# Optimization experiments

Hardware: AMD Instinct MI355X
Metric: run time of the kernel (lower is better)

Reference implementation:

```python
import jax, jax.numpy as jnp
import numpy as np

M, B, S, D, H = 8, 4, 512, 512, 8
HD = D // H  # head_dim = 64


def setup_inputs() -> dict:
    key = jax.random.key(0)
    k1, k2, k3 = jax.random.split(key, 3)
    x = jax.random.normal(k1, (M, B, S, D), dtype=jnp.float32)
    qkv_weight = jax.random.normal(k2, (M, D, 3 * D), dtype=jnp.float32) * 0.02
    proj_weight = jax.random.normal(k3, (M, D, D), dtype=jnp.float32) * 0.02
    return {"x": x, "qkv_weight": qkv_weight, "proj_weight": proj_weight}


def reference(x, qkv_weight, proj_weight):
    m, b, s, d = x.shape
    # model-axis batched QKV projection
    qkv = jnp.einsum('mbti,mio->mbto', x, qkv_weight)
    q, k, v = jnp.split(qkv, 3, axis=-1)
    # [m, b, h, s, hd]
    q = q.reshape(m, b, s, H, HD).transpose(0, 1, 3, 2, 4)
    k = k.reshape(m, b, s, H, HD).transpose(0, 1, 3, 2, 4)
    v = v.reshape(m, b, s, H, HD).transpose(0, 1, 3, 2, 4)
    att = jnp.einsum('mbhqd,mbhkd->mbhqk', q, k) / jnp.sqrt(jnp.float32(HD))
    causal = jnp.tril(jnp.ones((s, s), dtype=bool))
    att = jnp.where(causal, att, jnp.float32(-jnp.inf))
    att = jax.nn.softmax(att, axis=-1)
    y = jnp.einsum('mbhqk,mbhkd->mbhqd', att, v)
    y = y.transpose(0, 1, 3, 2, 4).reshape(m, b, s, d)
    return jnp.einsum('mbti,mio->mbto', y, proj_weight)
```

## Files before the change

### kernel.cpp

```cpp
#include <hip/hip_runtime.h>
#include <hip/hip_bf16.h>


typedef unsigned short u16;
typedef unsigned int u32;
typedef __attribute__((ext_vector_type(8))) short short8;
typedef __attribute__((ext_vector_type(4))) float f32x4;
typedef __attribute__((ext_vector_type(4))) unsigned short u16x4;
typedef __attribute__((ext_vector_type(8))) unsigned short u16x8;
typedef __attribute__((ext_vector_type(2))) unsigned int u32x2;

#define MFMA16(a, b, c) __builtin_amdgcn_mfma_f32_16x16x32_bf16((a), (b), (c), 0, 0, 0)

__device__ __forceinline__ u16 f2bf(float f) {
  union { __hip_bfloat16 h; u16 u; } cv;
  cv.h = __float2bfloat16(f);
  return cv.u;
}

__device__ __forceinline__ void gl_lds16(const u16* g, u16* l) {
  __builtin_amdgcn_global_load_lds(
      (const __attribute__((address_space(1))) void*)g,
      (__attribute__((address_space(3))) void*)l, 16, 0, 0);
}

__global__ __launch_bounds__(256) void xcast_kernel(const float* __restrict__ in,
                                                    u16* __restrict__ out, long n8) {
  long stride = (long)gridDim.x * 256;
  for (long i = blockIdx.x * 256L + threadIdx.x; i < n8; i += stride) {
    f32x4 a = *(const f32x4*)(in + i * 8);
    f32x4 b = *(const f32x4*)(in + i * 8 + 4);
    u16x8 o = {f2bf(a[0]), f2bf(a[1]), f2bf(a[2]), f2bf(a[3]),
               f2bf(b[0]), f2bf(b[1]), f2bf(b[2]), f2bf(b[3])};
    *(u16x8*)(out + i * 8) = o;
  }
}

__global__ __launch_bounds__(256) void wtrans_kernel(const float* __restrict__ in,
                                                     u16* __restrict__ out, int R, int C) {
  __shared__ float t[32][33];
  int m = blockIdx.z;
  const float* pin = in + (size_t)m * R * C;
  u16* pout = out + (size_t)m * R * C;
  int c0 = blockIdx.x * 32, r0 = blockIdx.y * 32;
  int tx = threadIdx.x, ty = threadIdx.y;
#pragma unroll
  for (int i = 0; i < 4; ++i) {
    int r = ty + i * 8;
    t[r][tx] = pin[(size_t)(r0 + r) * C + c0 + tx];
  }
  __syncthreads();
#pragma unroll
  for (int i = 0; i < 4; ++i) {
    int r = ty + i * 8;
    pout[(size_t)(c0 + r) * R + r0 + tx] = f2bf(t[tx][r]);
  }
}

__global__ __launch_bounds__(256) void qkv_gemm_kernel(const u16* __restrict__ XB,
                                                       const u16* __restrict__ WT,
                                                       u16* __restrict__ Q,
                                                       u16* __restrict__ K,
                                                       u16* __restrict__ VT) {
  __shared__ __attribute__((aligned(16))) u16 As[128 * 32];
  __shared__ __attribute__((aligned(16))) u16 Bs[128 * 32];
  int m = blockIdx.z;
  const u16* A = XB + (size_t)m * 2048 * 512;
  const u16* BT = WT + (size_t)m * 1536 * 512;
  int r0 = blockIdx.y * 128, c0 = blockIdx.x * 128;
  int t = threadIdx.x;
  int lane = t & 63, w = t >> 6;
  int wr = (w >> 1) * 64, wc = (w & 1) * 64;
  int fr = lane & 15, fc = lane >> 4;

  int u0 = w * 128 + lane;
  int u1 = w * 128 + 64 + lane;
  int ar0 = u0 >> 2, ak0 = (u0 & 3) * 8;
  int ar1 = u1 >> 2, ak1 = (u1 & 3) * 8;
  u16* lbase0 = &As[0] + (size_t)(w * 128) * 8;
  u16* lbase1 = &As[0] + (size_t)(w * 128 + 64) * 8;
  u16* lbb0 = &Bs[0] + (size_t)(w * 128) * 8;
  u16* lbb1 = &Bs[0] + (size_t)(w * 128 + 64) * 8;

  f32x4 acc[4][4];
#pragma unroll
  for (int i = 0; i < 4; ++i)
#pragma unroll
    for (int j = 0; j < 4; ++j) acc[i][j] = f32x4{0.f, 0.f, 0.f, 0.f};

  for (int kk = 0; kk < 512; kk += 32) {
    gl_lds16(A + (size_t)(r0 + ar0) * 512 + kk + ak0, lbase0);
    gl_lds16(A + (size_t)(r0 + ar1) * 512 + kk + ak1, lbase1);
    gl_lds16(BT + (size_t)(c0 + ar0) * 512 + kk + ak0, lbb0);
    gl_lds16(BT + (size_t)(c0 + ar1) * 512 + kk + ak1, lbb1);
    __syncthreads();
    short8 af[4], bf[4];
#pragma unroll
    for (int i = 0; i < 4; ++i) af[i] = *(const short8*)&As[(wr + i * 16 + fr) * 32 + fc * 8];
#pragma unroll
    for (int j = 0; j < 4; ++j) bf[j] = *(const short8*)&Bs[(wc + j * 16 + fr) * 32 + fc * 8];
#pragma unroll
    for (int i = 0; i < 4; ++i)
#pragma unroll
      for (int j = 0; j < 4; ++j) acc[i][j] = MFMA16(af[i], bf[j], acc[i][j]);
    __syncthreads();
  }

  int seg = c0 >> 9;
#pragma unroll
  for (int i = 0; i < 4; ++i) {
#pragma unroll
    for (int j = 0; j < 4; ++j) {
#pragma unroll
      for (int r = 0; r < 4; ++r) {
        int grow = r0 + wr + i * 16 + fc * 4 + r;
        int gcol = c0 + wc + j * 16 + fr;
        int b = grow >> 9, s = grow & 511;
        int cc = gcol & 511;
        int hh = cc >> 6, hd = cc & 63;
        size_t headoff = (size_t)((m * 4 + b) * 8 + hh) * 32768;
        u16 val = f2bf(acc[i][j][r]);
        if (seg == 0)      Q[headoff + s * 64 + hd] = val;
        else if (seg == 1) K[headoff + s * 64 + hd] = val;
        else               VT[headoff + hd * 512 + s] = val;
      }
    }
  }
}

__global__ __launch_bounds__(256) void attn_kernel(const u16* __restrict__ Qg,
                                                   const u16* __restrict__ Kg,
                                                   const u16* __restrict__ VTg,
                                                   u16* __restrict__ Yg) {
  __shared__ u16 Ks[2][64][72];
  __shared__ u16 Vs[2][64][72];
  __shared__ u16 Pl[4][16][72];
  int bid = blockIdx.x;
  int qt = bid >> 8;
  int g = bid & 255;
  int h = g & 7, mb = g >> 3;
  int t = threadIdx.x, lane = t & 63, w = t >> 6;
  int fr = lane & 15, fc = lane >> 4;
  size_t hoff = ((size_t)mb * 8 + h) * 32768;
  const u16* Q = Qg + hoff;
  const u16* K = Kg + hoff;
  const u16* V = VTg + hoff;
  int qrow = qt * 64 + w * 16 + fr;
  const float SC = 0.125f * 1.44269504088896340736f;

  short8 qf0 = *(const short8*)(Q + (size_t)qrow * 64 + fc * 8);
  short8 qf1 = *(const short8*)(Q + (size_t)qrow * 64 + 32 + fc * 8);

  f32x4 acc[4];
#pragma unroll
  for (int d = 0; d < 4; ++d) acc[d] = f32x4{0.f, 0.f, 0.f, 0.f};
  float mst = -1e30f, lst = 0.f;

  int u0 = 2 * t, u1 = 2 * t + 1;
  int kr0 = u0 >> 3, kc0 = (u0 & 7) * 8;
  int kr1 = u1 >> 3, kc1 = (u1 & 7) * 8;

  {
    u16x8 a0 = *(const u16x8*)(K + (size_t)kr0 * 64 + kc0);
    u16x8 a1 = *(const u16x8*)(K + (size_t)kr1 * 64 + kc1);
    u16x8 b0 = *(const u16x8*)(V + (size_t)kr0 * 512 + kc0);
    u16x8 b1 = *(const u16x8*)(V + (size_t)kr1 * 512 + kc1);
    *(u16x8*)&Ks[0][kr0][kc0] = a0;
    *(u16x8*)&Ks[0][kr1][kc1] = a1;
    *(u16x8*)&Vs[0][kr0][kc0] = b0;
    *(u16x8*)&Vs[0][kr1][kc1] = b1;
  }
  __syncthreads();

  for (int kt = 0; kt <= qt; ++kt) {
    int cur = kt & 1;
    bool pref = kt < qt;
    u16x8 nk0, nk1, nv0, nv1;
    if (pref) {
      int kbn = (kt + 1) * 64;
      nk0 = *(const u16x8*)(K + (size_t)(kbn + kr0) * 64 + kc0);
      nk1 = *(const u16x8*)(K + (size_t)(kbn + kr1) * 64 + kc1);
      nv0 = *(const u16x8*)(V + (size_t)kr0 * 512 + kbn + kc0);
      nv1 = *(const u16x8*)(V + (size_t)kr1 * 512 + kbn + kc1);
    }

    f32x4 st[4];
#pragma unroll
    for (int sub = 0; sub < 4; ++sub) {
      short8 kf0 = *(const short8*)&Ks[cur][sub * 16 + fr][fc * 8];
      short8 kf1 = *(const short8*)&Ks[cur][sub * 16 + fr][32 + fc * 8];
      f32x4 z = f32x4{0.f, 0.f, 0.f, 0.f};
      z = MFMA16(kf0, qf0, z);
      st[sub] = MFMA16(kf1, qf1, z);
    }

    float p[4][4];
    float mt = -3e30f;
    bool diag = (kt == qt);
    int qloc = w * 16 + fr;
#pragma unroll
    for (int sub = 0; sub < 4; ++sub)
#pragma unroll
      for (int r = 0; r < 4; ++r) {
        float v = st[sub][r] * SC;
        if (diag && (sub * 16 + fc * 4 + r) > qloc) v = -1e30f;
        p[sub][r] = v;
        mt = fmaxf(mt, v);
      }
    mt = fmaxf(mt, __shfl_xor(mt, 16));
    mt = fmaxf(mt, __shfl_xor(mt, 32));
    float mn = fmaxf(mst, mt);
    float al = __builtin_amdgcn_exp2f(mst - mn);
    mst = mn;
    float rs = 0.f;
#pragma unroll
    for (int sub = 0; sub < 4; ++sub)
#pragma unroll
      for (int r = 0; r < 4; ++r) {
        float e = __builtin_amdgcn_exp2f(p[sub][r] - mn);
        p[sub][r] = e;
        rs += e;
      }
    rs += __shfl_xor(rs, 16);
    rs += __shfl_xor(rs, 32);
    lst = lst * al + rs;
#pragma unroll
    for (int d = 0; d < 4; ++d) acc[d] *= al;

#pragma unroll
    for (int sub = 0; sub < 4; ++sub) {
      u32 lo = (u32)f2bf(p[sub][0]) | ((u32)f2bf(p[sub][1]) << 16);
      u32 hi = (u32)f2bf(p[sub][2]) | ((u32)f2bf(p[sub][3]) << 16);
      *(u32x2*)&Pl[w][fr][sub * 16 + fc * 4] = u32x2{lo, hi};
    }

#pragma unroll
    for (int dt = 0; dt < 4; ++dt)
#pragma unroll
      for (int kc = 0; kc < 2; ++kc) {
        short8 vf = *(const short8*)&Vs[cur][dt * 16 + fr][kc * 32 + fc * 8];
        short8 pb = *(const short8*)&Pl[w][fr][kc * 32 + fc * 8];
        acc[dt] = MFMA16(vf, pb, acc[dt]);
      }

    if (pref) {
      *(u16x8*)&Ks[cur ^ 1][kr0][kc0] = nk0;
      *(u16x8*)&Ks[cur ^ 1][kr1][kc1] = nk1;
      *(u16x8*)&Vs[cur ^ 1][kr0][kc0] = nv0;
      *(u16x8*)&Vs[cur ^ 1][kr1][kc1] = nv1;
    }
    __syncthreads();
  }

  float inv = 1.0f / lst;
#pragma unroll
  for (int dt = 0; dt < 4; ++dt) {
    u16x4 o = {f2bf(acc[dt][0] * inv), f2bf(acc[dt][1] * inv),
               f2bf(acc[dt][2] * inv), f2bf(acc[dt][3] * inv)};
    *(u16x4*)(Yg + ((size_t)mb * 512 + qrow) * 512 + h * 64 + dt * 16 + fc * 4) = o;
  }
}

__global__ __launch_bounds__(256) void proj_gemm_kernel(const u16* __restrict__ Y,
                                                        const u16* __restrict__ PT,
                                                        float* __restrict__ OUT) {
  __shared__ __attribute__((aligned(16))) u16 As[128 * 32];
  __shared__ __attribute__((aligned(16))) u16 Bs[128 * 32];
  int m = blockIdx.z;
  const u16* A = Y + (size_t)m * 2048 * 512;
  const u16* BT = PT + (size_t)m * 512 * 512;
  float* C = OUT + (size_t)m * 2048 * 512;
  int r0 = blockIdx.y * 128, c0 = blockIdx.x * 128;
  int t = threadIdx.x;
  int lane = t & 63, w = t >> 6;
  int wr = (w >> 1) * 64, wc = (w & 1) * 64;
  int fr = lane & 15, fc = lane >> 4;

  int u0 = w * 128 + lane;
  int u1 = w * 128 + 64 + lane;
  int ar0 = u0 >> 2, ak0 = (u0 & 3) * 8;
  int ar1 = u1 >> 2, ak1 = (u1 & 3) * 8;
  u16* lbase0 = &As[0] + (size_t)(w * 128) * 8;
  u16* lbase1 = &As[0] + (size_t)(w * 128 + 64) * 8;
  u16* lbb0 = &Bs[0] + (size_t)(w * 128) * 8;
  u16* lbb1 = &Bs[0] + (size_t)(w * 128 + 64) * 8;

  f32x4 acc[4][4];
#pragma unroll
  for (int i = 0; i < 4; ++i)
#pragma unroll
    for (int j = 0; j < 4; ++j) acc[i][j] = f32x4{0.f, 0.f, 0.f, 0.f};

  for (int kk = 0; kk < 512; kk += 32) {
    gl_lds16(A + (size_t)(r0 + ar0) * 512 + kk + ak0, lbase0);
    gl_lds16(A + (size_t)(r0 + ar1) * 512 + kk + ak1, lbase1);
    gl_lds16(BT + (size_t)(c0 + ar0) * 512 + kk + ak0, lbb0);
    gl_lds16(BT + (size_t)(c0 + ar1) * 512 + kk + ak1, lbb1);
    __syncthreads();
    short8 af[4], bf[4];
#pragma unroll
    for (int i = 0; i < 4; ++i) af[i] = *(const short8*)&As[(wr + i * 16 + fr) * 32 + fc * 8];
#pragma unroll
    for (int j = 0; j < 4; ++j) bf[j] = *(const short8*)&Bs[(wc + j * 16 + fr) * 32 + fc * 8];
#pragma unroll
    for (int i = 0; i < 4; ++i)
#pragma unroll
      for (int j = 0; j < 4; ++j) acc[i][j] = MFMA16(af[i], bf[j], acc[i][j]);
    __syncthreads();
  }
#pragma unroll
  for (int i = 0; i < 4; ++i)
#pragma unroll
    for (int j = 0; j < 4; ++j)
#pragma unroll
      for (int r = 0; r < 4; ++r) {
        int grow = r0 + wr + i * 16 + fc * 4 + r;
        int gcol = c0 + wc + j * 16 + fr;
        C[(size_t)grow * 512 + gcol] = acc[i][j][r];
      }
}

extern "C" void kernel_launch(void* const* d_in, const int* in_sizes, int n_in,
                              void* d_out, int out_size, void* d_ws, size_t ws_size,
                              hipStream_t stream) {
  const float* x = (const float*)d_in[0];
  const float* wqkv = (const float*)d_in[1];
  const float* wproj = (const float*)d_in[2];
  float* out = (float*)d_out;

  u16* p = (u16*)d_ws;
  u16* wqkvT = p;  p += (size_t)8 * 1536 * 512;
  u16* wprojT = p; p += (size_t)8 * 512 * 512;
  u16* qb = p;     p += (size_t)8388608;
  u16* kb = p;     p += (size_t)8388608;
  u16* vtb = p;    p += (size_t)8388608;
  u16* xyb = p;    p += (size_t)8388608;

  xcast_kernel<<<2048, 256, 0, stream>>>(x, xyb, (long)8 * 4 * 512 * 512 / 8);
  wtrans_kernel<<<dim3(48, 16, 8), dim3(32, 8), 0, stream>>>(wqkv, wqkvT, 512, 1536);
  wtrans_kernel<<<dim3(16, 16, 8), dim3(32, 8), 0, stream>>>(wproj, wprojT, 512, 512);
  qkv_gemm_kernel<<<dim3(12, 16, 8), 256, 0, stream>>>(xyb, wqkvT, qb, kb, vtb);
  attn_kernel<<<2048, 256, 0, stream>>>(qb, kb, vtb, xyb);
  proj_gemm_kernel<<<dim3(4, 16, 8), 256, 0, stream>>>(xyb, wprojT, out);
}
```

Before: 220.7 us.

## Double-buffer GEMM LDS tiles, enlarge to 256-row blocks, remap grid for XCD locality

Both the QKV and projection GEMMs now use 512-thread workgroups covering 256x128 output tiles, with double-buffered LDS so the next K-slice's global-to-LDS load is issued before computing the current one. The grid is flattened and block IDs are remapped so consecutive blocks of the same model index land on the same XCD, aiming for better L2 reuse. The intent is to hide load latency, cut one barrier per step, and improve cache locality. The cost is doubled LDS use and fewer, larger workgroups, which may lower occupancy.

```diff
diff --git a/kernel.cpp b/kernel.cpp
--- a/kernel.cpp
+++ b/kernel.cpp
@@ -57,30 +57,30 @@
   }
 }
 
-__global__ __launch_bounds__(256) void qkv_gemm_kernel(const u16* __restrict__ XB,
+__global__ __launch_bounds__(512) void qkv_gemm_kernel(const u16* __restrict__ XB,
                                                        const u16* __restrict__ WT,
                                                        u16* __restrict__ Q,
                                                        u16* __restrict__ K,
                                                        u16* __restrict__ VT) {
-  __shared__ __attribute__((aligned(16))) u16 As[128 * 32];
-  __shared__ __attribute__((aligned(16))) u16 Bs[128 * 32];
-  int m = blockIdx.z;
+  __shared__ __attribute__((aligned(16))) u16 As[2][256 * 32];
+  __shared__ __attribute__((aligned(16))) u16 Bs[2][128 * 32];
+  int bid = blockIdx.x;
+  int wgid = (bid & 7) * 96 + (bid >> 3);
+  int m = wgid / 96;
+  int rem = wgid % 96;
+  int r0 = (rem / 12) * 256, c0 = (rem % 12) * 128;
   const u16* A = XB + (size_t)m * 2048 * 512;
   const u16* BT = WT + (size_t)m * 1536 * 512;
-  int r0 = blockIdx.y * 128, c0 = blockIdx.x * 128;
   int t = threadIdx.x;
   int lane = t & 63, w = t >> 6;
   int wr = (w >> 1) * 64, wc = (w & 1) * 64;
   int fr = lane & 15, fc = lane >> 4;
 
-  int u0 = w * 128 + lane;
-  int u1 = w * 128 + 64 + lane;
-  int ar0 = u0 >> 2, ak0 = (u0 & 3) * 8;
-  int ar1 = u1 >> 2, ak1 = (u1 & 3) * 8;
-  u16* lbase0 = &As[0] + (size_t)(w * 128) * 8;
-  u16* lbase1 = &As[0] + (size_t)(w * 128 + 64) * 8;
-  u16* lbb0 = &Bs[0] + (size_t)(w * 128) * 8;
-  u16* lbb1 = &Bs[0] + (size_t)(w * 128 + 64) * 8;
+  int ar0 = t >> 2, ak0 = (t & 3) * 8;
+  int ar1 = (t + 512) >> 2, ak1 = ((t + 512) & 3) * 8;
+  u16* ldsA0[2] = {&As[0][(size_t)w * 64 * 8], &As[1][(size_t)w * 64 * 8]};
+  u16* ldsA1[2] = {&As[0][(size_t)(512 + w * 64) * 8], &As[1][(size_t)(512 + w * 64) * 8]};
+  u16* ldsB0[2] = {&Bs[0][(size_t)w * 64 * 8], &Bs[1][(size_t)w * 64 * 8]};
 
   f32x4 acc[4][4];
 #pragma unroll
@@ -88,21 +88,28 @@
 #pragma unroll
     for (int j = 0; j < 4; ++j) acc[i][j] = f32x4{0.f, 0.f, 0.f, 0.f};
 
-  for (int kk = 0; kk < 512; kk += 32) {
-    gl_lds16(A + (size_t)(r0 + ar0) * 512 + kk + ak0, lbase0);
-    gl_lds16(A + (size_t)(r0 + ar1) * 512 + kk + ak1, lbase1);
-    gl_lds16(BT + (size_t)(c0 + ar0) * 512 + kk + ak0, lbb0);
-    gl_lds16(BT + (size_t)(c0 + ar1) * 512 + kk + ak1, lbb1);
-    __syncthreads();
-    short8 af[4], bf[4];
-#pragma unroll
-    for (int i = 0; i < 4; ++i) af[i] = *(const short8*)&As[(wr + i * 16 + fr) * 32 + fc * 8];
-#pragma unroll
-    for (int j = 0; j < 4; ++j) bf[j] = *(const short8*)&Bs[(wc + j * 16 + fr) * 32 + fc * 8];
+  gl_lds16(A + (size_t)(r0 + ar0) * 512 + ak0, ldsA0[0]);
+  gl_lds16(A + (size_t)(r0 + ar1) * 512 + ak1, ldsA1[0]);
+  gl_lds16(BT + (size_t)(c0 + ar0) * 512 + ak0, ldsB0[0]);
+  __syncthreads();
+
+  for (int ks = 0; ks < 16; ++ks) {
+    int cur = ks & 1;
+    if (ks + 1 < 16) {
+      int kk = (ks + 1) * 32;
+      gl_lds16(A + (size_t)(r0 + ar0) * 512 + kk + ak0, ldsA0[cur ^ 1]);
+      gl_lds16(A + (size_t)(r0 + ar1) * 512 + kk + ak1, ldsA1[cur ^ 1]);
+      gl_lds16(BT + (size_t)(c0 + ar0) * 512 + kk + ak0, ldsB0[cur ^ 1]);
+    }
+    short8 af[4], bf_[4];
+#pragma unroll
+    for (int i = 0; i < 4; ++i) af[i] = *(const short8*)&As[cur][(wr + i * 16 + fr) * 32 + fc * 8];
+#pragma unroll
+    for (int j = 0; j < 4; ++j) bf_[j] = *(const short8*)&Bs[cur][(wc + j * 16 + fr) * 32 + fc * 8];
 #pragma unroll
     for (int i = 0; i < 4; ++i)
 #pragma unroll
-      for (int j = 0; j < 4; ++j) acc[i][j] = MFMA16(af[i], bf[j], acc[i][j]);
+      for (int j = 0; j < 4; ++j) acc[i][j] = MFMA16(af[i], bf_[j], acc[i][j]);
     __syncthreads();
   }
 
@@ -261,29 +268,29 @@
   }
 }
 
-__global__ __launch_bounds__(256) void proj_gemm_kernel(const u16* __restrict__ Y,
+__global__ __launch_bounds__(512) void proj_gemm_kernel(const u16* __restrict__ Y,
                                                         const u16* __restrict__ PT,
                                                         float* __restrict__ OUT) {
-  __shared__ __attribute__((aligned(16))) u16 As[128 * 32];
-  __shared__ __attribute__((aligned(16))) u16 Bs[128 * 32];
-  int m = blockIdx.z;
+  __shared__ __attribute__((aligned(16))) u16 As[2][256 * 32];
+  __shared__ __attribute__((aligned(16))) u16 Bs[2][128 * 32];
+  int bid = blockIdx.x;
+  int wgid = (bid & 7) * 32 + (bid >> 3);
+  int m = wgid / 32;
+  int rem = wgid % 32;
+  int r0 = (rem / 4) * 256, c0 = (rem % 4) * 128;
   const u16* A = Y + (size_t)m * 2048 * 512;
   const u16* BT = PT + (size_t)m * 512 * 512;
   float* C = OUT + (size_t)m * 2048 * 512;
-  int r0 = blockIdx.y * 128, c0 = blockIdx.x * 128;
   int t = threadIdx.x;
   int lane = t & 63, w = t >> 6;
   int wr = (w >> 1) * 64, wc = (w & 1) * 64;
   int fr = lane & 15, fc = lane >> 4;
 
-  int u0 = w * 128 + lane;
-  int u1 = w * 128 + 64 + lane;
-  int ar0 = u0 >> 2, ak0 = (u0 & 3) * 8;
-  int ar1 = u1 >> 2, ak1 = (u1 & 3) * 8;
-  u16* lbase0 = &As[0] + (size_t)(w * 128) * 8;
-  u16* lbase1 = &As[0] + (size_t)(w * 128 + 64) * 8;
-  u16* lbb0 = &Bs[0] + (size_t)(w * 128) * 8;
-  u16* lbb1 = &Bs[0] + (size_t)(w * 128 + 64) * 8;
+  int ar0 = t >> 2, ak0 = (t & 3) * 8;
+  int ar1 = (t + 512) >> 2, ak1 = ((t + 512) & 3) * 8;
+  u16* ldsA0[2] = {&As[0][(size_t)w * 64 * 8], &As[1][(size_t)w * 64 * 8]};
+  u16* ldsA1[2] = {&As[0][(size_t)(512 + w * 64) * 8], &As[1][(size_t)(512 + w * 64) * 8]};
+  u16* ldsB0[2] = {&Bs[0][(size_t)w * 64 * 8], &Bs[1][(size_t)w * 64 * 8]};
 
   f32x4 acc[4][4];
 #pragma unroll
@@ -291,21 +298,28 @@
 #pragma unroll
     for (int j = 0; j < 4; ++j) acc[i][j] = f32x4{0.f, 0.f, 0.f, 0.f};
 
-  for (int kk = 0; kk < 512; kk += 32) {
-    gl_lds16(A + (size_t)(r0 + ar0) * 512 + kk + ak0, lbase0);
-    gl_lds16(A + (size_t)(r0 + ar1) * 512 + kk + ak1, lbase1);
-    gl_lds16(BT + (size_t)(c0 + ar0) * 512 + kk + ak0, lbb0);
-    gl_lds16(BT + (size_t)(c0 + ar1) * 512 + kk + ak1, lbb1);
-    __syncthreads();
-    short8 af[4], bf[4];
-#pragma unroll
-    for (int i = 0; i < 4; ++i) af[i] = *(const short8*)&As[(wr + i * 16 + fr) * 32 + fc * 8];
-#pragma unroll
-    for (int j = 0; j < 4; ++j) bf[j] = *(const short8*)&Bs[(wc + j * 16 + fr) * 32 + fc * 8];
+  gl_lds16(A + (size_t)(r0 + ar0) * 512 + ak0, ldsA0[0]);
+  gl_lds16(A + (size_t)(r0 + ar1) * 512 + ak1, ldsA1[0]);
+  gl_lds16(BT + (size_t)(c0 + ar0) * 512 + ak0, ldsB0[0]);
+  __syncthreads();
+
+  for (int ks = 0; ks < 16; ++ks) {
+    int cur = ks & 1;
+    if (ks + 1 < 16) {
+      int kk = (ks + 1) * 32;
+      gl_lds16(A + (size_t)(r0 + ar0) * 512 + kk + ak0, ldsA0[cur ^ 1]);
+      gl_lds16(A + (size_t)(r0 + ar1) * 512 + kk + ak1, ldsA1[cur ^ 1]);
+      gl_lds16(BT + (size_t)(c0 + ar0) * 512 + kk + ak0, ldsB0[cur ^ 1]);
+    }
+    short8 af[4], bf_[4];
+#pragma unroll
+    for (int i = 0; i < 4; ++i) af[i] = *(const short8*)&As[cur][(wr + i * 16 + fr) * 32 + fc * 8];
+#pragma unroll
+    for (int j = 0; j < 4; ++j) bf_[j] = *(const short8*)&Bs[cur][(wc + j * 16 + fr) * 32 + fc * 8];
 #pragma unroll
     for (int i = 0; i < 4; ++i)
 #pragma unroll
-      for (int j = 0; j < 4; ++j) acc[i][j] = MFMA16(af[i], bf[j], acc[i][j]);
+      for (int j = 0; j < 4; ++j) acc[i][j] = MFMA16(af[i], bf_[j], acc[i][j]);
     __syncthreads();
   }
 #pragma unroll
@@ -339,7 +353,7 @@
   xcast_kernel<<<2048, 256, 0, stream>>>(x, xyb, (long)8 * 4 * 512 * 512 / 8);
   wtrans_kernel<<<dim3(48, 16, 8), dim3(32, 8), 0, stream>>>(wqkv, wqkvT, 512, 1536);
   wtrans_kernel<<<dim3(16, 16, 8), dim3(32, 8), 0, stream>>>(wproj, wprojT, 512, 512);
-  qkv_gemm_kernel<<<dim3(12, 16, 8), 256, 0, stream>>>(xyb, wqkvT, qb, kb, vtb);
+  qkv_gemm_kernel<<<768, 512, 0, stream>>>(xyb, wqkvT, qb, kb, vtb);
   attn_kernel<<<2048, 256, 0, stream>>>(qb, kb, vtb, xyb);
-  proj_gemm_kernel<<<dim3(4, 16, 8), 256, 0, stream>>>(xyb, wprojT, out);
-}
+  proj_gemm_kernel<<<256, 512, 0, stream>>>(xyb, wprojT, out);
+}
```

Result: no change. 219.9 us (-0.4%).

## Triple-buffer GEMM K-loop with async LDS loads, swizzle, and XCD-aware block mapping

Applied to the files above, without the earlier changes.

Rewrites the QKV and projection GEMM main loops to use three LDS buffers, prefetching two K-tiles ahead with a single barrier per iteration and explicit vmcnt waits. Global loads into LDS now use an XOR swizzle to reduce bank conflicts on the fragment reads. Blocks are launched as a 1D grid and remapped so that consecutive blocks on the same XCD share the same model index, which should improve L2 locality. The V-transposed epilogue now packs four bf16 values into one vector store. The cost is higher LDS use per block, which can lower occupancy.

```diff
diff --git a/kernel.cpp b/kernel.cpp
--- a/kernel.cpp
+++ b/kernel.cpp
@@ -62,25 +62,22 @@
                                                        u16* __restrict__ Q,
                                                        u16* __restrict__ K,
                                                        u16* __restrict__ VT) {
-  __shared__ __attribute__((aligned(16))) u16 As[128 * 32];
-  __shared__ __attribute__((aligned(16))) u16 Bs[128 * 32];
-  int m = blockIdx.z;
+  __shared__ __attribute__((aligned(16))) u16 As[3][128 * 32];
+  __shared__ __attribute__((aligned(16))) u16 Bs[3][128 * 32];
+  int bid = blockIdx.x;
+  int wgid = (bid & 7) * 192 + (bid >> 3);
+  int m = wgid / 192;
+  int rem = wgid % 192;
+  int r0 = (rem / 12) * 128, c0 = (rem % 12) * 128;
   const u16* A = XB + (size_t)m * 2048 * 512;
   const u16* BT = WT + (size_t)m * 1536 * 512;
-  int r0 = blockIdx.y * 128, c0 = blockIdx.x * 128;
   int t = threadIdx.x;
   int lane = t & 63, w = t >> 6;
   int wr = (w >> 1) * 64, wc = (w & 1) * 64;
   int fr = lane & 15, fc = lane >> 4;
 
-  int u0 = w * 128 + lane;
-  int u1 = w * 128 + 64 + lane;
-  int ar0 = u0 >> 2, ak0 = (u0 & 3) * 8;
-  int ar1 = u1 >> 2, ak1 = (u1 & 3) * 8;
-  u16* lbase0 = &As[0] + (size_t)(w * 128) * 8;
-  u16* lbase1 = &As[0] + (size_t)(w * 128 + 64) * 8;
-  u16* lbb0 = &Bs[0] + (size_t)(w * 128) * 8;
-  u16* lbb1 = &Bs[0] + (size_t)(w * 128 + 64) * 8;
+  int rA0 = t >> 2, cA0 = t & 3, sA0 = cA0 ^ ((rA0 >> 1) & 3);
+  int rA1 = (t + 256) >> 2, cA1 = t & 3, sA1 = cA1 ^ ((rA1 >> 1) & 3);
 
   f32x4 acc[4][4];
 #pragma unroll
@@ -88,43 +85,84 @@
 #pragma unroll
     for (int j = 0; j < 4; ++j) acc[i][j] = f32x4{0.f, 0.f, 0.f, 0.f};
 
-  for (int kk = 0; kk < 512; kk += 32) {
-    gl_lds16(A + (size_t)(r0 + ar0) * 512 + kk + ak0, lbase0);
-    gl_lds16(A + (size_t)(r0 + ar1) * 512 + kk + ak1, lbase1);
-    gl_lds16(BT + (size_t)(c0 + ar0) * 512 + kk + ak0, lbb0);
-    gl_lds16(BT + (size_t)(c0 + ar1) * 512 + kk + ak1, lbb1);
-    __syncthreads();
-    short8 af[4], bf[4];
-#pragma unroll
-    for (int i = 0; i < 4; ++i) af[i] = *(const short8*)&As[(wr + i * 16 + fr) * 32 + fc * 8];
-#pragma unroll
-    for (int j = 0; j < 4; ++j) bf[j] = *(const short8*)&Bs[(wc + j * 16 + fr) * 32 + fc * 8];
+#define QKV_STAGE(tile)                                                          \
+  {                                                                              \
+    int kk_ = (tile) * 32;                                                       \
+    int b_ = (tile) % 3;                                                         \
+    gl_lds16(A + (size_t)(r0 + rA0) * 512 + kk_ + sA0 * 8, &As[b_][w * 512]);    \
+    gl_lds16(A + (size_t)(r0 + rA1) * 512 + kk_ + sA1 * 8, &As[b_][2048 + w * 512]); \
+    gl_lds16(BT + (size_t)(c0 + rA0) * 512 + kk_ + sA0 * 8, &Bs[b_][w * 512]);   \
+    gl_lds16(BT + (size_t)(c0 + rA1) * 512 + kk_ + sA1 * 8, &Bs[b_][2048 + w * 512]); \
+  }
+
+#define QKV_COMPUTE(tile)                                                        \
+  {                                                                              \
+    int b_ = (tile) % 3;                                                         \
+    short8 af[4], bf_[4];                                                        \
+    _Pragma("unroll") for (int i = 0; i < 4; ++i) {                              \
+      int row = wr + i * 16 + fr;                                                \
+      int sl = fc ^ ((row >> 1) & 3);                                            \
+      af[i] = *(const short8*)&As[b_][row * 32 + sl * 8];                        \
+    }                                                                            \
+    _Pragma("unroll") for (int j = 0; j < 4; ++j) {                              \
+      int row = wc + j * 16 + fr;                                                \
+      int sl = fc ^ ((row >> 1) & 3);                                            \
+      bf_[j] = *(const short8*)&Bs[b_][row * 32 + sl * 8];                       \
+    }                                                                            \
+    _Pragma("unroll") for (int i = 0; i < 4; ++i)                                \
+      _Pragma("unroll") for (int j = 0; j < 4; ++j)                              \
+        acc[i][j] = MFMA16(af[i], bf_[j], acc[i][j]);                            \
+  }
+
+  QKV_STAGE(0);
+  QKV_STAGE(1);
+  for (int ks = 0; ks < 14; ++ks) {
+    asm volatile("s_waitcnt vmcnt(4)" ::: "memory");
+    __builtin_amdgcn_sched_barrier(0);
+    __builtin_amdgcn_s_barrier();
+    QKV_STAGE(ks + 2);
+    QKV_COMPUTE(ks);
+    __builtin_amdgcn_sched_barrier(0);
+  }
+  asm volatile("s_waitcnt vmcnt(0)" ::: "memory");
+  __builtin_amdgcn_sched_barrier(0);
+  __builtin_amdgcn_s_barrier();
+  QKV_COMPUTE(14);
+  QKV_COMPUTE(15);
+
+  int seg = c0 >> 9;
+  if (seg == 2) {
 #pragma unroll
     for (int i = 0; i < 4; ++i)
 #pragma unroll
-      for (int j = 0; j < 4; ++j) acc[i][j] = MFMA16(af[i], bf[j], acc[i][j]);
-    __syncthreads();
-  }
-
-  int seg = c0 >> 9;
-#pragma unroll
-  for (int i = 0; i < 4; ++i) {
-#pragma unroll
-    for (int j = 0; j < 4; ++j) {
-#pragma unroll
-      for (int r = 0; r < 4; ++r) {
-        int grow = r0 + wr + i * 16 + fc * 4 + r;
+      for (int j = 0; j < 4; ++j) {
+        int s0 = r0 + wr + i * 16 + fc * 4;
         int gcol = c0 + wc + j * 16 + fr;
-        int b = grow >> 9, s = grow & 511;
         int cc = gcol & 511;
         int hh = cc >> 6, hd = cc & 63;
+        int b = s0 >> 9, s = s0 & 511;
         size_t headoff = (size_t)((m * 4 + b) * 8 + hh) * 32768;
-        u16 val = f2bf(acc[i][j][r]);
-        if (seg == 0)      Q[headoff + s * 64 + hd] = val;
-        else if (seg == 1) K[headoff + s * 64 + hd] = val;
-        else               VT[headoff + hd * 512 + s] = val;
+        u16x4 pk = {f2bf(acc[i][j][0]), f2bf(acc[i][j][1]),
+                    f2bf(acc[i][j][2]), f2bf(acc[i][j][3])};
+        *(u16x4*)(VT + headoff + (size_t)hd * 512 + s) = pk;
       }
-    }
+  } else {
+#pragma unroll
+    for (int i = 0; i < 4; ++i)
+#pragma unroll
+      for (int j = 0; j < 4; ++j)
+#pragma unroll
+        for (int r = 0; r < 4; ++r) {
+          int grow = r0 + wr + i * 16 + fc * 4 + r;
+          int gcol = c0 + wc + j * 16 + fr;
+          int b = grow >> 9, s = grow & 511;
+          int cc = gcol & 511;
+          int hh = cc >> 6, hd = cc & 63;
+          size_t headoff = (size_t)((m * 4 + b) * 8 + hh) * 32768;
+          u16 val = f2bf(acc[i][j][r]);
+          if (seg == 0) Q[headoff + s * 64 + hd] = val;
+          else          K[headoff + s * 64 + hd] = val;
+        }
   }
 }
 
@@ -264,26 +302,23 @@
 __global__ __launch_bounds__(256) void proj_gemm_kernel(const u16* __restrict__ Y,
                                                         const u16* __restrict__ PT,
                                                         float* __restrict__ OUT) {
-  __shared__ __attribute__((aligned(16))) u16 As[128 * 32];
-  __shared__ __attribute__((aligned(16))) u16 Bs[128 * 32];
-  int m = blockIdx.z;
+  __shared__ __attribute__((aligned(16))) u16 As[3][128 * 32];
+  __shared__ __attribute__((aligned(16))) u16 Bs[3][128 * 32];
+  int bid = blockIdx.x;
+  int wgid = (bid & 7) * 64 + (bid >> 3);
+  int m = wgid / 64;
+  int rem = wgid % 64;
+  int r0 = (rem / 4) * 128, c0 = (rem % 4) * 128;
   const u16* A = Y + (size_t)m * 2048 * 512;
   const u16* BT = PT + (size_t)m * 512 * 512;
   float* C = OUT + (size_t)m * 2048 * 512;
-  int r0 = blockIdx.y * 128, c0 = blockIdx.x * 128;
   int t = threadIdx.x;
   int lane = t & 63, w = t >> 6;
   int wr = (w >> 1) * 64, wc = (w & 1) * 64;
   int fr = lane & 15, fc = lane >> 4;
 
-  int u0 = w * 128 + lane;
-  int u1 = w * 128 + 64 + lane;
-  int ar0 = u0 >> 2, ak0 = (u0 & 3) * 8;
-  int ar1 = u1 >> 2, ak1 = (u1 & 3) * 8;
-  u16* lbase0 = &As[0] + (size_t)(w * 128) * 8;
-  u16* lbase1 = &As[0] + (size_t)(w * 128 + 64) * 8;
-  u16* lbb0 = &Bs[0] + (size_t)(w * 128) * 8;
-  u16* lbb1 = &Bs[0] + (size_t)(w * 128 + 64) * 8;
+  int rA0 = t >> 2, sA0 = (t & 3) ^ ((rA0 >> 1) & 3);
+  int rA1 = (t + 256) >> 2, sA1 = (t & 3) ^ ((rA1 >> 1) & 3);
 
   f32x4 acc[4][4];
 #pragma unroll
@@ -291,23 +326,51 @@
 #pragma unroll
     for (int j = 0; j < 4; ++j) acc[i][j] = f32x4{0.f, 0.f, 0.f, 0.f};
 
-  for (int kk = 0; kk < 512; kk += 32) {
-    gl_lds16(A + (size_t)(r0 + ar0) * 512 + kk + ak0, lbase0);
-    gl_lds16(A + (size_t)(r0 + ar1) * 512 + kk + ak1, lbase1);
-    gl_lds16(BT + (size_t)(c0 + ar0) * 512 + kk + ak0, lbb0);
-    gl_lds16(BT + (size_t)(c0 + ar1) * 512 + kk + ak1, lbb1);
-    __syncthreads();
-    short8 af[4], bf[4];
-#pragma unroll
-    for (int i = 0; i < 4; ++i) af[i] = *(const short8*)&As[(wr + i * 16 + fr) * 32 + fc * 8];
-#pragma unroll
-    for (int j = 0; j < 4; ++j) bf[j] = *(const short8*)&Bs[(wc + j * 16 + fr) * 32 + fc * 8];
-#pragma unroll
-    for (int i = 0; i < 4; ++i)
-#pragma unroll
-      for (int j = 0; j < 4; ++j) acc[i][j] = MFMA16(af[i], bf[j], acc[i][j]);
-    __syncthreads();
-  }
+#define PROJ_STAGE(tile)                                                         \
+  {                                                                              \
+    int kk_ = (tile) * 32;                                                       \
+    int b_ = (tile) % 3;                                                         \
+    gl_lds16(A + (size_t)(r0 + rA0) * 512 + kk_ + sA0 * 8, &As[b_][w * 512]);    \
+    gl_lds16(A + (size_t)(r0 + rA1) * 512 + kk_ + sA1 * 8, &As[b_][2048 + w * 512]); \
+    gl_lds16(BT + (size_t)(c0 + rA0) * 512 + kk_ + sA0 * 8, &Bs[b_][w * 512]);   \
+    gl_lds16(BT + (size_t)(c0 + rA1) * 512 + kk_ + sA1 * 8, &Bs[b_][2048 + w * 512]); \
+  }
+
+#define PROJ_COMPUTE(tile)                                                       \
+  {                                                                              \
+    int b_ = (tile) % 3;                                                         \
+    short8 af[4], bf_[4];                                                        \
+    _Pragma("unroll") for (int i = 0; i < 4; ++i) {                              \
+      int row = wr + i * 16 + fr;                                                \
+      int sl = fc ^ ((row >> 1) & 3);                                            \
+      af[i] = *(const short8*)&As[b_][row * 32 + sl * 8];                        \
+    }                                                                            \
+    _Pragma("unroll") for (int j = 0; j < 4; ++j) {                              \
+      int row = wc + j * 16 + fr;                                                \
+      int sl = fc ^ ((row >> 1) & 3);                                            \
+      bf_[j] = *(const short8*)&Bs[b_][row * 32 + sl * 8];                       \
+    }                                                                            \
+    _Pragma("unroll") for (int i = 0; i < 4; ++i)                                \
+      _Pragma("unroll") for (int j = 0; j < 4; ++j)                              \
+        acc[i][j] = MFMA16(af[i], bf_[j], acc[i][j]);                            \
+  }
+
+  PROJ_STAGE(0);
+  PROJ_STAGE(1);
+  for (int ks = 0; ks < 14; ++ks) {
+    asm volatile("s_waitcnt vmcnt(4)" ::: "memory");
+    __builtin_amdgcn_sched_barrier(0);
+    __builtin_amdgcn_s_barrier();
+    PROJ_STAGE(ks + 2);
+    PROJ_COMPUTE(ks);
+    __builtin_amdgcn_sched_barrier(0);
+  }
+  asm volatile("s_waitcnt vmcnt(0)" ::: "memory");
+  __builtin_amdgcn_sched_barrier(0);
+  __builtin_amdgcn_s_barrier();
+  PROJ_COMPUTE(14);
+  PROJ_COMPUTE(15);
+
 #pragma unroll
   for (int i = 0; i < 4; ++i)
 #pragma unroll
@@ -339,7 +402,7 @@
   xcast_kernel<<<2048, 256, 0, stream>>>(x, xyb, (long)8 * 4 * 512 * 512 / 8);
   wtrans_kernel<<<dim3(48, 16, 8), dim3(32, 8), 0, stream>>>(wqkv, wqkvT, 512, 1536);
   wtrans_kernel<<<dim3(16, 16, 8), dim3(32, 8), 0, stream>>>(wproj, wprojT, 512, 512);
-  qkv_gemm_kernel<<<dim3(12, 16, 8), 256, 0, stream>>>(xyb, wqkvT, qb, kb, vtb);
+  qkv_gemm_kernel<<<1536, 256, 0, stream>>>(xyb, wqkvT, qb, kb, vtb);
   attn_kernel<<<2048, 256, 0, stream>>>(qb, kb, vtb, xyb);
-  proj_gemm_kernel<<<dim3(4, 16, 8), 256, 0, stream>>>(xyb, wprojT, out);
-}
+  proj_gemm_kernel<<<512, 256, 0, stream>>>(xyb, wprojT, out);
+}
```

Measured after the change: 191.5 us. -13.2%, faster.
